# Kernel optimization log

Measured on AMD Instinct MI355X. Metric: run time of the kernel, lower is better.

## Reference

```python
import jax, jax.numpy as jnp
import numpy as np

N_NODES = 10000
N_EDGES = 160000
IN_CH = 1030
HID = 256
HEADS = 4
OUT_CH = 49
NEG_SLOPE = 0.2
EPS = 1e-5


def setup_inputs() -> dict:
    key = jax.random.key(0)
    ks = jax.random.split(key, 20)
    HC = HID * HEADS  # 1024
    inp = {
        "x": jax.random.normal(ks[0], (N_NODES, IN_CH), dtype=jnp.float32),
        "edge_index": jax.random.randint(ks[1], (2, N_EDGES), 0, N_NODES, dtype=jnp.int64),
        # conv1 (GATv2): lin_l (source), lin_r (target), att, out bias
        "c1_wl": jax.random.normal(ks[2], (IN_CH, HC), dtype=jnp.float32) * 0.03,
        "c1_bl": jnp.zeros((HC,), dtype=jnp.float32),
        "c1_wr": jax.random.normal(ks[3], (IN_CH, HC), dtype=jnp.float32) * 0.03,
        "c1_br": jnp.zeros((HC,), dtype=jnp.float32),
        "c1_att": jax.random.normal(ks[4], (HEADS, HID), dtype=jnp.float32) * 0.06,
        "c1_bias": jnp.zeros((HC,), dtype=jnp.float32),
        # norm1 (per-node LayerNorm over channels)
        "ln1_w": jnp.ones((HC,), dtype=jnp.float32),
        "ln1_b": jnp.zeros((HC,), dtype=jnp.float32),
        # conv2
        "c2_wl": jax.random.normal(ks[5], (HC, HC), dtype=jnp.float32) * 0.03,
        "c2_bl": jnp.zeros((HC,), dtype=jnp.float32),
        "c2_wr": jax.random.normal(ks[6], (HC, HC), dtype=jnp.float32) * 0.03,
        "c2_br": jnp.zeros((HC,), dtype=jnp.float32),
        "c2_att": jax.random.normal(ks[7], (HEADS, HID), dtype=jnp.float32) * 0.06,
        "c2_bias": jnp.zeros((HC,), dtype=jnp.float32),
        # norm2
        "ln2_w": jnp.ones((HC,), dtype=jnp.float32),
        "ln2_b": jnp.zeros((HC,), dtype=jnp.float32),
        # classifier: Linear(HC, HID) -> ELU -> Linear(HID, OUT_CH)
        "cls_w1": jax.random.normal(ks[8], (HC, HID), dtype=jnp.float32) * 0.03,
        "cls_b1": jnp.zeros((HID,), dtype=jnp.float32),
        "cls_w2": jax.random.normal(ks[9], (HID, OUT_CH), dtype=jnp.float32) * 0.06,
        "cls_b2": jnp.zeros((OUT_CH,), dtype=jnp.float32),
    }
    return inp


def gatv2_conv(x, src, dst, wl, bl, wr, br, att, bias, n_nodes):
    """PyG GATv2Conv, concat heads. src/dst include self loops."""
    H, C = att.shape
    xl = (x @ wl + bl).reshape(-1, H, C)  # source transform [N,H,C]
    xr = (x @ wr + br).reshape(-1, H, C)  # target transform [N,H,C]
    m = xl[src] + xr[dst]                  # [E,H,C] gather + add
    e = jnp.einsum("ehc,hc->eh", jax.nn.leaky_relu(m, NEG_SLOPE), att)  # [E,H]
    # segment softmax over destination node
    emax = jax.ops.segment_max(e, dst, num_segments=n_nodes)
    p = jnp.exp(e - emax[dst])
    denom = jax.ops.segment_sum(p, dst, num_segments=n_nodes)
    alpha = p / (denom[dst] + 1e-16)       # [E,H]
    out = jax.ops.segment_sum(xl[src] * alpha[:, :, None], dst, num_segments=n_nodes)
    return out.reshape(n_nodes, H * C) + bias


def layer_norm(x, w, b):
    mu = jnp.mean(x, axis=-1, keepdims=True)
    var = jnp.var(x, axis=-1, keepdims=True)
    return (x - mu) / jnp.sqrt(var + EPS) * w + b


def reference(x, edge_index, c1_wl, c1_bl, c1_wr, c1_br, c1_att, c1_bias,
              ln1_w, ln1_b, c2_wl, c2_bl, c2_wr, c2_br, c2_att, c2_bias,
              ln2_w, ln2_b, cls_w1, cls_b1, cls_w2, cls_b2):
    n = x.shape[0]
    loops = jnp.arange(n, dtype=edge_index.dtype)
    src = jnp.concatenate([edge_index[0], loops])  # add_self_loops=True
    dst = jnp.concatenate([edge_index[1], loops])

    h = gatv2_conv(x, src, dst, c1_wl, c1_bl, c1_wr, c1_br, c1_att, c1_bias, n)
    h = jax.nn.elu(layer_norm(h, ln1_w, ln1_b))
    # dropout: identity at inference
    h = gatv2_conv(h, src, dst, c2_wl, c2_bl, c2_wr, c2_br, c2_att, c2_bias, n)
    h = jax.nn.elu(layer_norm(h, ln2_w, ln2_b))
    h = jax.nn.elu(h @ cls_w1 + cls_b1)
    return h @ cls_w2 + cls_b2  # [N, 49]
```

## Files before the change

### kernel.cpp

```cpp
#include <hip/hip_runtime.h>
#include <stdint.h>

#define N_NODES 10000
#define N_EDGES 160000
#define E_TOT   170000
#define IN_CH   1030
#define HC      1024
#define OUT_CH  49
#define NEG_SLOPE 0.2f
#define LN_EPS 1e-5f
#define LOG2E 1.4426950408889634f

#define MPAD  10112
#define K1PAD 1088

typedef __attribute__((ext_vector_type(8))) __bf16 bf16x8;
typedef __attribute__((ext_vector_type(4))) float floatx4;
typedef __attribute__((ext_vector_type(2))) float floatx2;
typedef _Float16 h2 __attribute__((ext_vector_type(2)));

static __device__ __forceinline__ unsigned short f2bf(float f) {
  union { float f; uint32_t u; } v; v.f = f;
  uint32_t u = v.u;
  u += 0x7fffu + ((u >> 16) & 1u);
  return (unsigned short)(u >> 16);
}
static __device__ __forceinline__ unsigned short f2h(float f) {
  _Float16 h = (_Float16)f;
  union { _Float16 h; unsigned short u; } v; v.h = h; return v.u;
}
static __device__ __forceinline__ h2 bits2h2(uint32_t u) {
  union { uint32_t i; h2 h; } v; v.i = u; return v.h;
}
static __device__ __forceinline__ floatx2 h2f2(h2 a) {
  floatx2 r; r.x = (float)a.x; r.y = (float)a.y; return r;
}


__global__ void cast_x_kernel(const float* __restrict__ x, unsigned short* __restrict__ xa,
                              int* __restrict__ counts, int* __restrict__ cursor) {
  int idx = blockIdx.x * 256 + threadIdx.x;
  if (idx < N_NODES) { counts[idx] = 0; cursor[idx] = 0; }
  if (idx >= N_NODES * K1PAD) return;
  int m = idx / K1PAD, k = idx - m * K1PAD;
  float v = (k < IN_CH) ? x[m * IN_CH + k] : 0.f;
  xa[idx] = f2bf(v);
}

__global__ void transpose_cast_kernel(const float* __restrict__ wa, const float* __restrict__ wb,
                                      int split, int lda, int ldb,
                                      int Kvalid, int Kout, unsigned short* __restrict__ out) {
  __shared__ float tile[32][33];
  int n0 = blockIdx.x * 32, k0 = blockIdx.y * 32;
  int tx = threadIdx.x, ty = threadIdx.y;
#pragma unroll
  for (int i = 0; i < 4; i++) {
    int k = k0 + ty + i * 8;
    int n = n0 + tx;
    float v = 0.f;
    if (k < Kvalid) v = (n < split) ? wa[(size_t)k * lda + n] : wb[(size_t)k * ldb + (n - split)];
    tile[ty + i * 8][tx] = v;
  }
  __syncthreads();
#pragma unroll
  for (int i = 0; i < 4; i++) {
    int n = n0 + ty + i * 8;
    int k = k0 + tx;
    out[(size_t)n * Kout + k] = f2bf(tile[tx][ty + i * 8]);
  }
}


__global__ void count_kernel(const int* __restrict__ dstArr, int* __restrict__ counts) {
  int e = blockIdx.x * 256 + threadIdx.x;
  if (e >= E_TOT) return;
  int d = (e < N_EDGES) ? dstArr[e] : (e - N_EDGES);
  atomicAdd(&counts[d], 1);
}

__global__ __launch_bounds__(256) void scan_kernel(const int* __restrict__ counts,
                                                   int* __restrict__ rstart) {
  __shared__ int sm[256];
  int t = threadIdx.x;
  int b0 = t * 40;
  int b1 = b0 + 40; if (b1 > N_NODES) b1 = N_NODES; if (b0 > N_NODES) b0 = N_NODES;
  int s = 0;
  for (int i = b0; i < b1; i++) s += counts[i];
  sm[t] = s; __syncthreads();
  for (int st = 1; st < 256; st <<= 1) {
    int add = (t >= st) ? sm[t - st] : 0;
    __syncthreads();
    sm[t] += add;
    __syncthreads();
  }
  int run = sm[t] - s;
  for (int i = b0; i < b1; i++) { rstart[i] = run; run += counts[i]; }
  if (t == 255) rstart[N_NODES] = run;
}

__global__ void scatter_kernel(const int* __restrict__ srcArr, const int* __restrict__ dstArr,
                               const int* __restrict__ row_start,
                               int* __restrict__ cursor, int* __restrict__ csrsrc) {
  int e = blockIdx.x * 256 + threadIdx.x;
  if (e >= E_TOT) return;
  int d, sv;
  if (e < N_EDGES) { d = dstArr[e]; sv = srcArr[e]; }
  else { d = e - N_EDGES; sv = d; }
  int pos = atomicAdd(&cursor[d], 1);
  csrsrc[row_start[d] + pos] = sv;
}

template <int MODE, int KC>
__global__ __launch_bounds__(256, 4) void gemm_bf16(
    const unsigned short* __restrict__ A, const unsigned short* __restrict__ Bt,
    float* __restrict__ Cf, unsigned short* __restrict__ Cb,
    const float* __restrict__ blo, const float* __restrict__ bhi,
    int M, int ldc, int bsplit)
{
  __shared__ __align__(16) unsigned short As[128 * 64];
  __shared__ __align__(16) unsigned short Bs[128 * 64];
  const int t = threadIdx.x;
  const int w = t >> 6, lane = t & 63;
  const int tile_n = blockIdx.x * 128, tile_m = blockIdx.y * 128;

  floatx4 acc[4][4] = {};

  const int q = w * 64 + lane;
  const int row0 = q >> 3;
  const int gj = (q & 7) ^ (row0 & 7);
  const unsigned short* gA0 = A  + (size_t)(tile_m + row0) * KC + gj * 8;
  const unsigned short* gB0 = Bt + (size_t)(tile_n + row0) * KC + gj * 8;

  const int wm = (w >> 1) * 64, wn = (w & 1) * 64;
  const int lrow = lane & 15, cg0 = (lane >> 4);
  const int sw = lrow & 7;

#pragma unroll 1
  for (int k0 = 0; k0 < KC; k0 += 64) {
#pragma unroll
    for (int p = 0; p < 4; p++) {
      __builtin_amdgcn_global_load_lds(
          (const __attribute__((address_space(1))) void*)(gA0 + p * 32 * KC),
          (__attribute__((address_space(3))) void*)(As + p * 2048 + w * 512), 16, 0, 0);
      __builtin_amdgcn_global_load_lds(
          (const __attribute__((address_space(1))) void*)(gB0 + p * 32 * KC),
          (__attribute__((address_space(3))) void*)(Bs + p * 2048 + w * 512), 16, 0, 0);
    }
    gA0 += 64; gB0 += 64;
    __syncthreads();
#pragma unroll
    for (int h = 0; h < 2; h++) {
      const int sc = (h * 4 + cg0) ^ sw;
      bf16x8 a[4], b[4];
#pragma unroll
      for (int mi = 0; mi < 4; mi++)
        a[mi] = *(const bf16x8*)(As + (wm + mi * 16 + lrow) * 64 + sc * 8);
#pragma unroll
      for (int ni = 0; ni < 4; ni++)
        b[ni] = *(const bf16x8*)(Bs + (wn + ni * 16 + lrow) * 64 + sc * 8);
#pragma unroll
      for (int mi = 0; mi < 4; mi++)
#pragma unroll
        for (int ni = 0; ni < 4; ni++)
          acc[mi][ni] = __builtin_amdgcn_mfma_f32_16x16x32_bf16(a[mi], b[ni], acc[mi][ni], 0, 0, 0);
    }
    __syncthreads();
  }

  const int rbase = (lane >> 4) * 4;
#pragma unroll
  for (int mi = 0; mi < 4; mi++) {
#pragma unroll
    for (int r = 0; r < 4; r++) {
      int m = tile_m + wm + mi * 16 + rbase + r;
      if (m >= M) continue;
#pragma unroll
      for (int ni = 0; ni < 4; ni++) {
        int n = tile_n + wn + ni * 16 + lrow;
        float v = acc[mi][ni][r] + (n < bsplit ? blo[n] : bhi[n - bsplit]);
        if (MODE == 0) {
          Cf[(size_t)m * ldc + n] = v;
        } else if (MODE == 1) {
          Cf[(size_t)m * ldc + n] = v > 0.f ? v : expm1f(v);
        } else {
          Cb[(size_t)m * 2048 + n] = f2h(v);
        }
      }
    }
  }
}


__global__ __launch_bounds__(256) void gat_ln_kernel(
    const unsigned short* __restrict__ xlr,
    const float* __restrict__ att,
    const int* __restrict__ csrsrc, const int* __restrict__ rstart,
    const float* __restrict__ bias,
    const float* __restrict__ lnw, const float* __restrict__ lnb,
    unsigned short* __restrict__ out)
{
  const int d = blockIdx.x;
  const int t = threadIdx.x;
  const int lane = t & 63, wv = t >> 6;
  const int c = wv * 256 + lane * 4;

  uint2 xru = *(const uint2*)(xlr + (size_t)d * 2048 + 1024 + c);
  h2 xr0 = bits2h2(xru.x), xr1 = bits2h2(xru.y);
  float4 aw4 = *(const float4*)(att + c);
  h2 aw0, aw1;
  aw0.x = (_Float16)(aw4.x * LOG2E); aw0.y = (_Float16)(aw4.y * LOG2E);
  aw1.x = (_Float16)(aw4.z * LOG2E); aw1.y = (_Float16)(aw4.w * LOG2E);
  const h2 ns = {(_Float16)NEG_SLOPE, (_Float16)NEG_SLOPE};
  const unsigned short* xbase = xlr + c;

  int start = rstart[d], deg = rstart[d + 1] - start;

  float m = -3.0e38f, l = 0.f;
  floatx2 accA = {0.f, 0.f}, accB = {0.f, 0.f};

  int i = 0;
  for (; i + 4 <= deg; i += 4) {
    int s0 = csrsrc[start + i],     s1 = csrsrc[start + i + 1];
    int s2 = csrsrc[start + i + 2], s3 = csrsrc[start + i + 3];
    uint2 u0 = *(const uint2*)(xbase + (size_t)s0 * 2048);
    uint2 u1 = *(const uint2*)(xbase + (size_t)s1 * 2048);
    uint2 u2 = *(const uint2*)(xbase + (size_t)s2 * 2048);
    uint2 u3 = *(const uint2*)(xbase + (size_t)s3 * 2048);
    h2 xh0a = bits2h2(u0.x), xh0b = bits2h2(u0.y);
    h2 xh1a = bits2h2(u1.x), xh1b = bits2h2(u1.y);
    h2 xh2a = bits2h2(u2.x), xh2b = bits2h2(u2.y);
    h2 xh3a = bits2h2(u3.x), xh3b = bits2h2(u3.y);
    h2 t0a = xh0a + xr0, t0b = xh0b + xr1;
    h2 t1a = xh1a + xr0, t1b = xh1b + xr1;
    h2 t2a = xh2a + xr0, t2b = xh2b + xr1;
    h2 t3a = xh3a + xr0, t3b = xh3b + xr1;
    h2 r0a = __builtin_elementwise_max(t0a, t0a * ns);
    h2 r0b = __builtin_elementwise_max(t0b, t0b * ns);
    h2 r1a = __builtin_elementwise_max(t1a, t1a * ns);
    h2 r1b = __builtin_elementwise_max(t1b, t1b * ns);
    h2 r2a = __builtin_elementwise_max(t2a, t2a * ns);
    h2 r2b = __builtin_elementwise_max(t2b, t2b * ns);
    h2 r3a = __builtin_elementwise_max(t3a, t3a * ns);
    h2 r3b = __builtin_elementwise_max(t3b, t3b * ns);
    float p0 = __builtin_amdgcn_fdot2(r0b, aw1, __builtin_amdgcn_fdot2(r0a, aw0, 0.f, false), false);
    float p1 = __builtin_amdgcn_fdot2(r1b, aw1, __builtin_amdgcn_fdot2(r1a, aw0, 0.f, false), false);
    float p2 = __builtin_amdgcn_fdot2(r2b, aw1, __builtin_amdgcn_fdot2(r2a, aw0, 0.f, false), false);
    float p3 = __builtin_amdgcn_fdot2(r3b, aw1, __builtin_amdgcn_fdot2(r3a, aw0, 0.f, false), false);
#pragma unroll
    for (int mm = 32; mm >= 1; mm >>= 1) {
      p0 += __shfl_xor(p0, mm, 64);
      p1 += __shfl_xor(p1, mm, 64);
      p2 += __shfl_xor(p2, mm, 64);
      p3 += __shfl_xor(p3, mm, 64);
    }
    float mx = fmaxf(fmaxf(p0, p1), fmaxf(p2, p3));
    if (mx > m) {
      float sc = exp2f(m - mx);
      floatx2 scv; scv.x = sc; scv.y = sc;
      accA *= scv; accB *= scv; l *= sc;
      m = mx;
    }
    float pe0 = exp2f(p0 - m), pe1 = exp2f(p1 - m);
    float pe2 = exp2f(p2 - m), pe3 = exp2f(p3 - m);
    floatx2 x0A = h2f2(xh0a), x0B = h2f2(xh0b);
    floatx2 x1A = h2f2(xh1a), x1B = h2f2(xh1b);
    floatx2 x2A = h2f2(xh2a), x2B = h2f2(xh2b);
    floatx2 x3A = h2f2(xh3a), x3B = h2f2(xh3b);
    floatx2 v0; v0.x = pe0; v0.y = pe0;
    floatx2 v1; v1.x = pe1; v1.y = pe1;
    floatx2 v2; v2.x = pe2; v2.y = pe2;
    floatx2 v3; v3.x = pe3; v3.y = pe3;
    accA += x0A * v0; accA += x1A * v1; accA += x2A * v2; accA += x3A * v3;
    accB += x0B * v0; accB += x1B * v1; accB += x2B * v2; accB += x3B * v3;
    l += pe0 + pe1 + pe2 + pe3;
  }
  for (; i < deg; i++) {
    int s0 = csrsrc[start + i];
    uint2 u0 = *(const uint2*)(xbase + (size_t)s0 * 2048);
    h2 xh0a = bits2h2(u0.x), xh0b = bits2h2(u0.y);
    h2 t0a = xh0a + xr0, t0b = xh0b + xr1;
    h2 r0a = __builtin_elementwise_max(t0a, t0a * ns);
    h2 r0b = __builtin_elementwise_max(t0b, t0b * ns);
    float p0 = __builtin_amdgcn_fdot2(r0b, aw1, __builtin_amdgcn_fdot2(r0a, aw0, 0.f, false), false);
#pragma unroll
    for (int mm = 32; mm >= 1; mm >>= 1) p0 += __shfl_xor(p0, mm, 64);
    if (p0 > m) {
      float sc = exp2f(m - p0);
      floatx2 scv; scv.x = sc; scv.y = sc;
      accA *= scv; accB *= scv; l *= sc;
      m = p0;
    }
    float pe0 = exp2f(p0 - m);
    floatx2 x0A = h2f2(xh0a), x0B = h2f2(xh0b);
    floatx2 pe0v; pe0v.x = pe0; pe0v.y = pe0;
    accA += x0A * pe0v;
    accB += x0B * pe0v;
    l += pe0;
  }

  float rd = 1.f / (l + 1e-16f);
  float4 bv = *(const float4*)(bias + c);
  float o0 = accA.x * rd + bv.x, o1 = accA.y * rd + bv.y;
  float o2 = accB.x * rd + bv.z, o3 = accB.y * rd + bv.w;

  __shared__ float ws1[4], ws2[4];
  float s1 = o0 + o1 + o2 + o3;
  float s2 = o0 * o0 + o1 * o1 + o2 * o2 + o3 * o3;
#pragma unroll
  for (int mm = 32; mm >= 1; mm >>= 1) {
    s1 += __shfl_xor(s1, mm, 64);
    s2 += __shfl_xor(s2, mm, 64);
  }
  if (lane == 0) { ws1[wv] = s1; ws2[wv] = s2; }
  __syncthreads();
  float mean = (ws1[0] + ws1[1] + ws1[2] + ws1[3]) * (1.f / 1024.f);
  float var  = (ws2[0] + ws2[1] + ws2[2] + ws2[3]) * (1.f / 1024.f) - mean * mean;
  float rstd = rsqrtf(var + LN_EPS);
  float4 wv4 = *(const float4*)(lnw + c);
  float4 bb  = *(const float4*)(lnb + c);
  float z0 = (o0 - mean) * rstd * wv4.x + bb.x; z0 = z0 > 0.f ? z0 : expm1f(z0);
  float z1 = (o1 - mean) * rstd * wv4.y + bb.y; z1 = z1 > 0.f ? z1 : expm1f(z1);
  float z2 = (o2 - mean) * rstd * wv4.z + bb.z; z2 = z2 > 0.f ? z2 : expm1f(z2);
  float z3 = (o3 - mean) * rstd * wv4.w + bb.w; z3 = z3 > 0.f ? z3 : expm1f(z3);
  ushort4 u;
  u.x = f2bf(z0); u.y = f2bf(z1); u.z = f2bf(z2); u.w = f2bf(z3);
  *(ushort4*)(out + (size_t)d * 1024 + c) = u;
}


__global__ __launch_bounds__(64) void cls2_kernel(
    const float* __restrict__ h3, const float* __restrict__ w2,
    const float* __restrict__ b2, float* __restrict__ out)
{
  __shared__ float row[256];
  int node = blockIdx.x, t = threadIdx.x;
  *(float4*)(row + t * 4) = *(const float4*)(h3 + (size_t)node * 256 + t * 4);
  __syncthreads();
  if (t < OUT_CH) {
    float a0 = 0.f, a1 = 0.f, a2 = 0.f, a3 = 0.f;
#pragma unroll 4
    for (int k = 0; k < 256; k += 4) {
      float4 r = *(const float4*)(row + k);
      a0 += r.x * w2[(k + 0) * OUT_CH + t];
      a1 += r.y * w2[(k + 1) * OUT_CH + t];
      a2 += r.z * w2[(k + 2) * OUT_CH + t];
      a3 += r.w * w2[(k + 3) * OUT_CH + t];
    }
    out[node * OUT_CH + t] = (a0 + a1) + (a2 + a3) + b2[t];
  }
}


extern "C" void kernel_launch(void* const* d_in, const int* in_sizes, int n_in,
                              void* d_out, int out_size, void* d_ws, size_t ws_size,
                              hipStream_t stream)
{
  const float* x       = (const float*)d_in[0];
  const int*   ei      = (const int*)d_in[1];
  const float* c1_wl   = (const float*)d_in[2];
  const float* c1_bl   = (const float*)d_in[3];
  const float* c1_wr   = (const float*)d_in[4];
  const float* c1_br   = (const float*)d_in[5];
  const float* c1_att  = (const float*)d_in[6];
  const float* c1_bias = (const float*)d_in[7];
  const float* ln1_w   = (const float*)d_in[8];
  const float* ln1_b   = (const float*)d_in[9];
  const float* c2_wl   = (const float*)d_in[10];
  const float* c2_bl   = (const float*)d_in[11];
  const float* c2_wr   = (const float*)d_in[12];
  const float* c2_br   = (const float*)d_in[13];
  const float* c2_att  = (const float*)d_in[14];
  const float* c2_bias = (const float*)d_in[15];
  const float* ln2_w   = (const float*)d_in[16];
  const float* ln2_b   = (const float*)d_in[17];
  const float* cls_w1  = (const float*)d_in[18];
  const float* cls_b1  = (const float*)d_in[19];
  const float* cls_w2  = (const float*)d_in[20];
  const float* cls_b2  = (const float*)d_in[21];

  const int* srcArr = ei;
  const int* dstArr = ei + N_EDGES;

  char* ws = (char*)d_ws;
  size_t off = 0;
  auto alloc = [&](size_t bytes) { void* p = ws + off; off += (bytes + 255) & ~(size_t)255; return p; };
  unsigned short* xa      = (unsigned short*)alloc((size_t)MPAD * K1PAD * 2);
  unsigned short* wt1     = (unsigned short*)alloc((size_t)2048 * K1PAD * 2);
  unsigned short* wt2     = (unsigned short*)alloc((size_t)2048 * 1024 * 2);
  unsigned short* wtc1    = (unsigned short*)alloc((size_t)256 * 1024 * 2);
  unsigned short* xlr     = (unsigned short*)alloc((size_t)N_NODES * 2048 * 2);
  float*          h3      = (float*)alloc((size_t)N_NODES * 256 * 4);
  unsigned short* hb      = (unsigned short*)alloc((size_t)MPAD * 1024 * 2);
  int*            counts  = (int*)alloc(N_NODES * 4);
  int*            cursor  = (int*)alloc(N_NODES * 4);
  int*            rstart  = (int*)alloc((N_NODES + 1) * 4);
  int*            csrsrc  = (int*)alloc(E_TOT * 4);
  (void)in_sizes; (void)n_in; (void)out_size; (void)ws_size;

  cast_x_kernel<<<(N_NODES * K1PAD + 255) / 256, 256, 0, stream>>>(x, xa, counts, cursor);
  transpose_cast_kernel<<<dim3(64, 34), dim3(32, 8), 0, stream>>>(c1_wl, c1_wr, 1024, 1024, 1024, IN_CH, K1PAD, wt1);
  transpose_cast_kernel<<<dim3(64, 32), dim3(32, 8), 0, stream>>>(c2_wl, c2_wr, 1024, 1024, 1024, 1024, 1024, wt2);
  transpose_cast_kernel<<<dim3(8, 32), dim3(32, 8), 0, stream>>>(cls_w1, cls_w1, 256, 256, 256, 1024, 1024, wtc1);

  count_kernel<<<(E_TOT + 255) / 256, 256, 0, stream>>>(dstArr, counts);
  scan_kernel<<<1, 256, 0, stream>>>(counts, rstart);
  scatter_kernel<<<(E_TOT + 255) / 256, 256, 0, stream>>>(srcArr, dstArr, rstart, cursor, csrsrc);

  gemm_bf16<2, K1PAD><<<dim3(16, 79), 256, 0, stream>>>(xa, wt1, nullptr, xlr, c1_bl, c1_br, N_NODES, 0, 1024);
  gat_ln_kernel<<<N_NODES, 256, 0, stream>>>(xlr, c1_att, csrsrc, rstart, c1_bias, ln1_w, ln1_b, hb);

  gemm_bf16<2, 1024><<<dim3(16, 79), 256, 0, stream>>>(hb, wt2, nullptr, xlr, c2_bl, c2_br, N_NODES, 0, 1024);
  gat_ln_kernel<<<N_NODES, 256, 0, stream>>>(xlr, c2_att, csrsrc, rstart, c2_bias, ln2_w, ln2_b, hb);

  gemm_bf16<1, 1024><<<dim3(2, 79), 256, 0, stream>>>(hb, wtc1, h3, nullptr, cls_b1, cls_b1, N_NODES, 256, 1024);
  cls2_kernel<<<N_NODES, 64, 0, stream>>>(h3, cls_w2, cls_b2, (float*)d_out);
}
```

Baseline: 500.3 us.

## Process four edges in parallel per wavefront with 16-lane groups in GAT aggregation

Restructures the GATv2 aggregation+LayerNorm kernel so that each wavefront splits into four 16-lane groups. Each group handles a different edge, and each lane covers 16 channels with 128-bit loads instead of 4 channels with 64-bit loads. This shortens the per-edge cross-lane reduction from 6 to 4 shuffle steps and prefetches the next source index. Groups run independent online softmaxes that are merged with shuffles at the end, and only group 0 writes the output. The cost is higher register use (16 accumulators per lane), a final merge step, and divergence on the rescale branch.

```diff
diff --git a/kernel.cpp b/kernel.cpp
--- a/kernel.cpp
+++ b/kernel.cpp
@@ -202,129 +202,166 @@
   const int d = blockIdx.x;
   const int t = threadIdx.x;
   const int lane = t & 63, wv = t >> 6;
-  const int c = wv * 256 + lane * 4;
-
-  uint2 xru = *(const uint2*)(xlr + (size_t)d * 2048 + 1024 + c);
-  h2 xr0 = bits2h2(xru.x), xr1 = bits2h2(xru.y);
-  float4 aw4 = *(const float4*)(att + c);
-  h2 aw0, aw1;
-  aw0.x = (_Float16)(aw4.x * LOG2E); aw0.y = (_Float16)(aw4.y * LOG2E);
-  aw1.x = (_Float16)(aw4.z * LOG2E); aw1.y = (_Float16)(aw4.w * LOG2E);
+  const int g  = lane >> 4;
+  const int li = lane & 15;
+  const int c = wv * 256 + li * 16;
+
+  const unsigned short* xrp = xlr + (size_t)d * 2048 + 1024 + c;
+  uint4 xru0 = *(const uint4*)(xrp);
+  uint4 xru1 = *(const uint4*)(xrp + 8);
+  h2 xr[8];
+  xr[0] = bits2h2(xru0.x); xr[1] = bits2h2(xru0.y);
+  xr[2] = bits2h2(xru0.z); xr[3] = bits2h2(xru0.w);
+  xr[4] = bits2h2(xru1.x); xr[5] = bits2h2(xru1.y);
+  xr[6] = bits2h2(xru1.z); xr[7] = bits2h2(xru1.w);
+
+  float4 a0 = *(const float4*)(att + c);
+  float4 a1 = *(const float4*)(att + c + 4);
+  float4 a2 = *(const float4*)(att + c + 8);
+  float4 a3 = *(const float4*)(att + c + 12);
+  h2 aw[8];
+  aw[0].x = (_Float16)(a0.x * LOG2E); aw[0].y = (_Float16)(a0.y * LOG2E);
+  aw[1].x = (_Float16)(a0.z * LOG2E); aw[1].y = (_Float16)(a0.w * LOG2E);
+  aw[2].x = (_Float16)(a1.x * LOG2E); aw[2].y = (_Float16)(a1.y * LOG2E);
+  aw[3].x = (_Float16)(a1.z * LOG2E); aw[3].y = (_Float16)(a1.w * LOG2E);
+  aw[4].x = (_Float16)(a2.x * LOG2E); aw[4].y = (_Float16)(a2.y * LOG2E);
+  aw[5].x = (_Float16)(a2.z * LOG2E); aw[5].y = (_Float16)(a2.w * LOG2E);
+  aw[6].x = (_Float16)(a3.x * LOG2E); aw[6].y = (_Float16)(a3.y * LOG2E);
+  aw[7].x = (_Float16)(a3.z * LOG2E); aw[7].y = (_Float16)(a3.w * LOG2E);
   const h2 ns = {(_Float16)NEG_SLOPE, (_Float16)NEG_SLOPE};
+
   const unsigned short* xbase = xlr + c;
-
-  int start = rstart[d], deg = rstart[d + 1] - start;
+  const int start = rstart[d], end = rstart[d + 1];
 
   float m = -3.0e38f, l = 0.f;
-  floatx2 accA = {0.f, 0.f}, accB = {0.f, 0.f};
-
-  int i = 0;
-  for (; i + 4 <= deg; i += 4) {
-    int s0 = csrsrc[start + i],     s1 = csrsrc[start + i + 1];
-    int s2 = csrsrc[start + i + 2], s3 = csrsrc[start + i + 3];
-    uint2 u0 = *(const uint2*)(xbase + (size_t)s0 * 2048);
-    uint2 u1 = *(const uint2*)(xbase + (size_t)s1 * 2048);
-    uint2 u2 = *(const uint2*)(xbase + (size_t)s2 * 2048);
-    uint2 u3 = *(const uint2*)(xbase + (size_t)s3 * 2048);
-    h2 xh0a = bits2h2(u0.x), xh0b = bits2h2(u0.y);
-    h2 xh1a = bits2h2(u1.x), xh1b = bits2h2(u1.y);
-    h2 xh2a = bits2h2(u2.x), xh2b = bits2h2(u2.y);
-    h2 xh3a = bits2h2(u3.x), xh3b = bits2h2(u3.y);
-    h2 t0a = xh0a + xr0, t0b = xh0b + xr1;
-    h2 t1a = xh1a + xr0, t1b = xh1b + xr1;
-    h2 t2a = xh2a + xr0, t2b = xh2b + xr1;
-    h2 t3a = xh3a + xr0, t3b = xh3b + xr1;
-    h2 r0a = __builtin_elementwise_max(t0a, t0a * ns);
-    h2 r0b = __builtin_elementwise_max(t0b, t0b * ns);
-    h2 r1a = __builtin_elementwise_max(t1a, t1a * ns);
-    h2 r1b = __builtin_elementwise_max(t1b, t1b * ns);
-    h2 r2a = __builtin_elementwise_max(t2a, t2a * ns);
-    h2 r2b = __builtin_elementwise_max(t2b, t2b * ns);
-    h2 r3a = __builtin_elementwise_max(t3a, t3a * ns);
-    h2 r3b = __builtin_elementwise_max(t3b, t3b * ns);
-    float p0 = __builtin_amdgcn_fdot2(r0b, aw1, __builtin_amdgcn_fdot2(r0a, aw0, 0.f, false), false);
-    float p1 = __builtin_amdgcn_fdot2(r1b, aw1, __builtin_amdgcn_fdot2(r1a, aw0, 0.f, false), false);
-    float p2 = __builtin_amdgcn_fdot2(r2b, aw1, __builtin_amdgcn_fdot2(r2a, aw0, 0.f, false), false);
-    float p3 = __builtin_amdgcn_fdot2(r3b, aw1, __builtin_amdgcn_fdot2(r3a, aw0, 0.f, false), false);
-#pragma unroll
-    for (int mm = 32; mm >= 1; mm >>= 1) {
-      p0 += __shfl_xor(p0, mm, 64);
-      p1 += __shfl_xor(p1, mm, 64);
-      p2 += __shfl_xor(p2, mm, 64);
-      p3 += __shfl_xor(p3, mm, 64);
-    }
-    float mx = fmaxf(fmaxf(p0, p1), fmaxf(p2, p3));
-    if (mx > m) {
-      float sc = exp2f(m - mx);
+  floatx2 acc[8] = {};
+
+  int eq0 = start + g;
+  int s_next = csrsrc[(eq0 < end) ? eq0 : start];
+
+  for (int i = start; i < end; i += 4) {
+    const int scur = s_next;
+    const bool valid = (i + g) < end;
+    const int eqn = i + 4 + g;
+    s_next = csrsrc[(eqn < end) ? eqn : start];
+
+    const unsigned short* xp = xbase + (size_t)scur * 2048;
+    uint4 u0 = *(const uint4*)(xp);
+    uint4 u1 = *(const uint4*)(xp + 8);
+    h2 xh[8];
+    xh[0] = bits2h2(u0.x); xh[1] = bits2h2(u0.y);
+    xh[2] = bits2h2(u0.z); xh[3] = bits2h2(u0.w);
+    xh[4] = bits2h2(u1.x); xh[5] = bits2h2(u1.y);
+    xh[6] = bits2h2(u1.z); xh[7] = bits2h2(u1.w);
+
+    float pa = 0.f, pb = 0.f;
+#pragma unroll
+    for (int j = 0; j < 4; j++) {
+      h2 tj = xh[j] + xr[j];
+      h2 rj = __builtin_elementwise_max(tj, tj * ns);
+      pa = __builtin_amdgcn_fdot2(rj, aw[j], pa, false);
+      h2 tk = xh[j + 4] + xr[j + 4];
+      h2 rk = __builtin_elementwise_max(tk, tk * ns);
+      pb = __builtin_amdgcn_fdot2(rk, aw[j + 4], pb, false);
+    }
+    float p = pa + pb;
+    p += __shfl_xor(p, 1, 64);
+    p += __shfl_xor(p, 2, 64);
+    p += __shfl_xor(p, 4, 64);
+    p += __shfl_xor(p, 8, 64);
+
+    const float mnew = fmaxf(m, p);
+    const float pe = valid ? exp2f(p - mnew) : 0.f;
+    if (__any(valid && (p > m))) {
+      const float sc = exp2f(m - mnew);
       floatx2 scv; scv.x = sc; scv.y = sc;
-      accA *= scv; accB *= scv; l *= sc;
-      m = mx;
-    }
-    float pe0 = exp2f(p0 - m), pe1 = exp2f(p1 - m);
-    float pe2 = exp2f(p2 - m), pe3 = exp2f(p3 - m);
-    floatx2 x0A = h2f2(xh0a), x0B = h2f2(xh0b);
-    floatx2 x1A = h2f2(xh1a), x1B = h2f2(xh1b);
-    floatx2 x2A = h2f2(xh2a), x2B = h2f2(xh2b);
-    floatx2 x3A = h2f2(xh3a), x3B = h2f2(xh3b);
-    floatx2 v0; v0.x = pe0; v0.y = pe0;
-    floatx2 v1; v1.x = pe1; v1.y = pe1;
-    floatx2 v2; v2.x = pe2; v2.y = pe2;
-    floatx2 v3; v3.x = pe3; v3.y = pe3;
-    accA += x0A * v0; accA += x1A * v1; accA += x2A * v2; accA += x3A * v3;
-    accB += x0B * v0; accB += x1B * v1; accB += x2B * v2; accB += x3B * v3;
-    l += pe0 + pe1 + pe2 + pe3;
-  }
-  for (; i < deg; i++) {
-    int s0 = csrsrc[start + i];
-    uint2 u0 = *(const uint2*)(xbase + (size_t)s0 * 2048);
-    h2 xh0a = bits2h2(u0.x), xh0b = bits2h2(u0.y);
-    h2 t0a = xh0a + xr0, t0b = xh0b + xr1;
-    h2 r0a = __builtin_elementwise_max(t0a, t0a * ns);
-    h2 r0b = __builtin_elementwise_max(t0b, t0b * ns);
-    float p0 = __builtin_amdgcn_fdot2(r0b, aw1, __builtin_amdgcn_fdot2(r0a, aw0, 0.f, false), false);
-#pragma unroll
-    for (int mm = 32; mm >= 1; mm >>= 1) p0 += __shfl_xor(p0, mm, 64);
-    if (p0 > m) {
-      float sc = exp2f(m - p0);
-      floatx2 scv; scv.x = sc; scv.y = sc;
-      accA *= scv; accB *= scv; l *= sc;
-      m = p0;
-    }
-    float pe0 = exp2f(p0 - m);
-    floatx2 x0A = h2f2(xh0a), x0B = h2f2(xh0b);
-    floatx2 pe0v; pe0v.x = pe0; pe0v.y = pe0;
-    accA += x0A * pe0v;
-    accB += x0B * pe0v;
-    l += pe0;
-  }
-
-  float rd = 1.f / (l + 1e-16f);
-  float4 bv = *(const float4*)(bias + c);
-  float o0 = accA.x * rd + bv.x, o1 = accA.y * rd + bv.y;
-  float o2 = accB.x * rd + bv.z, o3 = accB.y * rd + bv.w;
+#pragma unroll
+      for (int j = 0; j < 8; j++) acc[j] *= scv;
+      l *= sc;
+      m = mnew;
+    }
+#pragma unroll
+    for (int j = 0; j < 8; j++) {
+      acc[j].x += (float)xh[j].x * pe;
+      acc[j].y += (float)xh[j].y * pe;
+    }
+    l += pe;
+  }
+
+  float M = m;
+  M = fmaxf(M, __shfl_xor(M, 16, 64));
+  M = fmaxf(M, __shfl_xor(M, 32, 64));
+  const float sc = exp2f(m - M);
+  l *= sc;
+  l += __shfl_xor(l, 16, 64);
+  l += __shfl_xor(l, 32, 64);
+  floatx2 scv; scv.x = sc; scv.y = sc;
+#pragma unroll
+  for (int j = 0; j < 8; j++) {
+    acc[j] *= scv;
+    acc[j].x += __shfl_xor(acc[j].x, 16, 64);
+    acc[j].y += __shfl_xor(acc[j].y, 16, 64);
+    acc[j].x += __shfl_xor(acc[j].x, 32, 64);
+    acc[j].y += __shfl_xor(acc[j].y, 32, 64);
+  }
+
+  const float rd = 1.f / (l + 1e-16f);
+  float4 b0 = *(const float4*)(bias + c);
+  float4 b1 = *(const float4*)(bias + c + 4);
+  float4 b2 = *(const float4*)(bias + c + 8);
+  float4 b3 = *(const float4*)(bias + c + 12);
+  float o[16];
+  o[0]  = acc[0].x * rd + b0.x; o[1]  = acc[0].y * rd + b0.y;
+  o[2]  = acc[1].x * rd + b0.z; o[3]  = acc[1].y * rd + b0.w;
+  o[4]  = acc[2].x * rd + b1.x; o[5]  = acc[2].y * rd + b1.y;
+  o[6]  = acc[3].x * rd + b1.z; o[7]  = acc[3].y * rd + b1.w;
+  o[8]  = acc[4].x * rd + b2.x; o[9]  = acc[4].y * rd + b2.y;
+  o[10] = acc[5].x * rd + b2.z; o[11] = acc[5].y * rd + b2.w;
+  o[12] = acc[6].x * rd + b3.x; o[13] = acc[6].y * rd + b3.y;
+  o[14] = acc[7].x * rd + b3.z; o[15] = acc[7].y * rd + b3.w;
 
   __shared__ float ws1[4], ws2[4];
-  float s1 = o0 + o1 + o2 + o3;
-  float s2 = o0 * o0 + o1 * o1 + o2 * o2 + o3 * o3;
-#pragma unroll
-  for (int mm = 32; mm >= 1; mm >>= 1) {
-    s1 += __shfl_xor(s1, mm, 64);
-    s2 += __shfl_xor(s2, mm, 64);
-  }
+  float s1 = 0.f, s2 = 0.f;
+#pragma unroll
+  for (int j = 0; j < 16; j++) { s1 += o[j]; s2 += o[j] * o[j]; }
+  s1 += __shfl_xor(s1, 1, 64); s2 += __shfl_xor(s2, 1, 64);
+  s1 += __shfl_xor(s1, 2, 64); s2 += __shfl_xor(s2, 2, 64);
+  s1 += __shfl_xor(s1, 4, 64); s2 += __shfl_xor(s2, 4, 64);
+  s1 += __shfl_xor(s1, 8, 64); s2 += __shfl_xor(s2, 8, 64);
   if (lane == 0) { ws1[wv] = s1; ws2[wv] = s2; }
   __syncthreads();
-  float mean = (ws1[0] + ws1[1] + ws1[2] + ws1[3]) * (1.f / 1024.f);
-  float var  = (ws2[0] + ws2[1] + ws2[2] + ws2[3]) * (1.f / 1024.f) - mean * mean;
-  float rstd = rsqrtf(var + LN_EPS);
-  float4 wv4 = *(const float4*)(lnw + c);
-  float4 bb  = *(const float4*)(lnb + c);
-  float z0 = (o0 - mean) * rstd * wv4.x + bb.x; z0 = z0 > 0.f ? z0 : expm1f(z0);
-  float z1 = (o1 - mean) * rstd * wv4.y + bb.y; z1 = z1 > 0.f ? z1 : expm1f(z1);
-  float z2 = (o2 - mean) * rstd * wv4.z + bb.z; z2 = z2 > 0.f ? z2 : expm1f(z2);
-  float z3 = (o3 - mean) * rstd * wv4.w + bb.w; z3 = z3 > 0.f ? z3 : expm1f(z3);
-  ushort4 u;
-  u.x = f2bf(z0); u.y = f2bf(z1); u.z = f2bf(z2); u.w = f2bf(z3);
-  *(ushort4*)(out + (size_t)d * 1024 + c) = u;
+  const float mean = (ws1[0] + ws1[1] + ws1[2] + ws1[3]) * (1.f / 1024.f);
+  const float var  = (ws2[0] + ws2[1] + ws2[2] + ws2[3]) * (1.f / 1024.f) - mean * mean;
+  const float rstd = rsqrtf(var + LN_EPS);
+
+  if (g == 0) {
+    float4 w0 = *(const float4*)(lnw + c);
+    float4 w1 = *(const float4*)(lnw + c + 4);
+    float4 w2 = *(const float4*)(lnw + c + 8);
+    float4 w3 = *(const float4*)(lnw + c + 12);
+    float4 q0 = *(const float4*)(lnb + c);
+    float4 q1 = *(const float4*)(lnb + c + 4);
+    float4 q2 = *(const float4*)(lnb + c + 8);
+    float4 q3 = *(const float4*)(lnb + c + 12);
+    float lw[16] = {w0.x,w0.y,w0.z,w0.w, w1.x,w1.y,w1.z,w1.w,
+                    w2.x,w2.y,w2.z,w2.w, w3.x,w3.y,w3.z,w3.w};
+    float lb[16] = {q0.x,q0.y,q0.z,q0.w, q1.x,q1.y,q1.z,q1.w,
+                    q2.x,q2.y,q2.z,q2.w, q3.x,q3.y,q3.z,q3.w};
+    uint32_t zz[16];
+#pragma unroll
+    for (int j = 0; j < 16; j++) {
+      float z = (o[j] - mean) * rstd * lw[j] + lb[j];
+      z = z > 0.f ? z : expm1f(z);
+      zz[j] = (uint32_t)f2bf(z);
+    }
+    uint4 v0, v1;
+    v0.x = zz[0]  | (zz[1]  << 16); v0.y = zz[2]  | (zz[3]  << 16);
+    v0.z = zz[4]  | (zz[5]  << 16); v0.w = zz[6]  | (zz[7]  << 16);
+    v1.x = zz[8]  | (zz[9]  << 16); v1.y = zz[10] | (zz[11] << 16);
+    v1.z = zz[12] | (zz[13] << 16); v1.w = zz[14] | (zz[15] << 16);
+    *(uint4*)(out + (size_t)d * 1024 + c) = v0;
+    *(uint4*)(out + (size_t)d * 1024 + c + 8) = v1;
+  }
 }
 
 
```

Result: slower. 550.2 us (+10.0%).

## Software-pipeline GAT neighbor gathers and remap GEMM workgroups per XCD

Applied to the files above, without the earlier changes.

The GAT aggregation loop now prefetches the next group of neighbor feature rows and the index group after that, overlapping gather latency with the softmax and accumulate math. The CSR index array is padded with 16 zeroed entries so the look-ahead reads stay in bounds. The GEMM workgroup-to-tile mapping is remapped so that blocks sharing an XCD get contiguous tiles, to improve L2 locality. This adds register pressure and some redundant prefetch loads at the tail.

```diff
diff --git a/kernel.cpp b/kernel.cpp
--- a/kernel.cpp
+++ b/kernel.cpp
@@ -102,7 +102,10 @@
                                const int* __restrict__ row_start,
                                int* __restrict__ cursor, int* __restrict__ csrsrc) {
   int e = blockIdx.x * 256 + threadIdx.x;
-  if (e >= E_TOT) return;
+  if (e >= E_TOT) {
+    return;
+  }
+  if (e < 16) csrsrc[E_TOT + e] = 0;
   int d, sv;
   if (e < N_EDGES) { d = dstArr[e]; sv = srcArr[e]; }
   else { d = e - N_EDGES; sv = d; }
@@ -121,13 +124,19 @@
   __shared__ __align__(16) unsigned short Bs[128 * 64];
   const int t = threadIdx.x;
   const int w = t >> 6, lane = t & 63;
-  const int tile_n = blockIdx.x * 128, tile_m = blockIdx.y * 128;
+
+  const unsigned int nwg = gridDim.x * gridDim.y;
+  const unsigned int bid = blockIdx.y * gridDim.x + blockIdx.x;
+  const unsigned int q8 = nwg >> 3, r8 = nwg & 7;
+  const unsigned int xcd = bid & 7, sub = bid >> 3;
+  const unsigned int wg = (xcd < r8 ? xcd * (q8 + 1) : r8 * (q8 + 1) + (xcd - r8) * q8) + sub;
+  const int tile_n = (wg % gridDim.x) * 128, tile_m = (wg / gridDim.x) * 128;
 
   floatx4 acc[4][4] = {};
 
-  const int q = w * 64 + lane;
-  const int row0 = q >> 3;
-  const int gj = (q & 7) ^ (row0 & 7);
+  const int qq = w * 64 + lane;
+  const int row0 = qq >> 3;
+  const int gj = (qq & 7) ^ (row0 & 7);
   const unsigned short* gA0 = A  + (size_t)(tile_m + row0) * KC + gj * 8;
   const unsigned short* gB0 = Bt + (size_t)(tile_n + row0) * KC + gj * 8;
 
@@ -219,60 +228,74 @@
   floatx2 accA = {0.f, 0.f}, accB = {0.f, 0.f};
 
   int i = 0;
-  for (; i + 4 <= deg; i += 4) {
-    int s0 = csrsrc[start + i],     s1 = csrsrc[start + i + 1];
-    int s2 = csrsrc[start + i + 2], s3 = csrsrc[start + i + 3];
-    uint2 u0 = *(const uint2*)(xbase + (size_t)s0 * 2048);
-    uint2 u1 = *(const uint2*)(xbase + (size_t)s1 * 2048);
-    uint2 u2 = *(const uint2*)(xbase + (size_t)s2 * 2048);
-    uint2 u3 = *(const uint2*)(xbase + (size_t)s3 * 2048);
-    h2 xh0a = bits2h2(u0.x), xh0b = bits2h2(u0.y);
-    h2 xh1a = bits2h2(u1.x), xh1b = bits2h2(u1.y);
-    h2 xh2a = bits2h2(u2.x), xh2b = bits2h2(u2.y);
-    h2 xh3a = bits2h2(u3.x), xh3b = bits2h2(u3.y);
-    h2 t0a = xh0a + xr0, t0b = xh0b + xr1;
-    h2 t1a = xh1a + xr0, t1b = xh1b + xr1;
-    h2 t2a = xh2a + xr0, t2b = xh2b + xr1;
-    h2 t3a = xh3a + xr0, t3b = xh3b + xr1;
-    h2 r0a = __builtin_elementwise_max(t0a, t0a * ns);
-    h2 r0b = __builtin_elementwise_max(t0b, t0b * ns);
-    h2 r1a = __builtin_elementwise_max(t1a, t1a * ns);
-    h2 r1b = __builtin_elementwise_max(t1b, t1b * ns);
-    h2 r2a = __builtin_elementwise_max(t2a, t2a * ns);
-    h2 r2b = __builtin_elementwise_max(t2b, t2b * ns);
-    h2 r3a = __builtin_elementwise_max(t3a, t3a * ns);
-    h2 r3b = __builtin_elementwise_max(t3b, t3b * ns);
-    float p0 = __builtin_amdgcn_fdot2(r0b, aw1, __builtin_amdgcn_fdot2(r0a, aw0, 0.f, false), false);
-    float p1 = __builtin_amdgcn_fdot2(r1b, aw1, __builtin_amdgcn_fdot2(r1a, aw0, 0.f, false), false);
-    float p2 = __builtin_amdgcn_fdot2(r2b, aw1, __builtin_amdgcn_fdot2(r2a, aw0, 0.f, false), false);
-    float p3 = __builtin_amdgcn_fdot2(r3b, aw1, __builtin_amdgcn_fdot2(r3a, aw0, 0.f, false), false);
-#pragma unroll
-    for (int mm = 32; mm >= 1; mm >>= 1) {
-      p0 += __shfl_xor(p0, mm, 64);
-      p1 += __shfl_xor(p1, mm, 64);
-      p2 += __shfl_xor(p2, mm, 64);
-      p3 += __shfl_xor(p3, mm, 64);
-    }
-    float mx = fmaxf(fmaxf(p0, p1), fmaxf(p2, p3));
-    if (mx > m) {
-      float sc = exp2f(m - mx);
-      floatx2 scv; scv.x = sc; scv.y = sc;
-      accA *= scv; accB *= scv; l *= sc;
-      m = mx;
-    }
-    float pe0 = exp2f(p0 - m), pe1 = exp2f(p1 - m);
-    float pe2 = exp2f(p2 - m), pe3 = exp2f(p3 - m);
-    floatx2 x0A = h2f2(xh0a), x0B = h2f2(xh0b);
-    floatx2 x1A = h2f2(xh1a), x1B = h2f2(xh1b);
-    floatx2 x2A = h2f2(xh2a), x2B = h2f2(xh2b);
-    floatx2 x3A = h2f2(xh3a), x3B = h2f2(xh3b);
-    floatx2 v0; v0.x = pe0; v0.y = pe0;
-    floatx2 v1; v1.x = pe1; v1.y = pe1;
-    floatx2 v2; v2.x = pe2; v2.y = pe2;
-    floatx2 v3; v3.x = pe3; v3.y = pe3;
-    accA += x0A * v0; accA += x1A * v1; accA += x2A * v2; accA += x3A * v3;
-    accB += x0B * v0; accB += x1B * v1; accB += x2B * v2; accB += x3B * v3;
-    l += pe0 + pe1 + pe2 + pe3;
+  if (deg >= 4) {
+    int sA0 = csrsrc[start],     sA1 = csrsrc[start + 1];
+    int sA2 = csrsrc[start + 2], sA3 = csrsrc[start + 3];
+    uint2 uA0 = *(const uint2*)(xbase + (size_t)sA0 * 2048);
+    uint2 uA1 = *(const uint2*)(xbase + (size_t)sA1 * 2048);
+    uint2 uA2 = *(const uint2*)(xbase + (size_t)sA2 * 2048);
+    uint2 uA3 = *(const uint2*)(xbase + (size_t)sA3 * 2048);
+    int sB0 = csrsrc[start + 4], sB1 = csrsrc[start + 5];
+    int sB2 = csrsrc[start + 6], sB3 = csrsrc[start + 7];
+    for (; i + 4 <= deg; i += 4) {
+      int sC0 = csrsrc[start + i + 8],  sC1 = csrsrc[start + i + 9];
+      int sC2 = csrsrc[start + i + 10], sC3 = csrsrc[start + i + 11];
+      uint2 uB0 = *(const uint2*)(xbase + (size_t)sB0 * 2048);
+      uint2 uB1 = *(const uint2*)(xbase + (size_t)sB1 * 2048);
+      uint2 uB2 = *(const uint2*)(xbase + (size_t)sB2 * 2048);
+      uint2 uB3 = *(const uint2*)(xbase + (size_t)sB3 * 2048);
+
+      h2 xh0a = bits2h2(uA0.x), xh0b = bits2h2(uA0.y);
+      h2 xh1a = bits2h2(uA1.x), xh1b = bits2h2(uA1.y);
+      h2 xh2a = bits2h2(uA2.x), xh2b = bits2h2(uA2.y);
+      h2 xh3a = bits2h2(uA3.x), xh3b = bits2h2(uA3.y);
+      h2 t0a = xh0a + xr0, t0b = xh0b + xr1;
+      h2 t1a = xh1a + xr0, t1b = xh1b + xr1;
+      h2 t2a = xh2a + xr0, t2b = xh2b + xr1;
+      h2 t3a = xh3a + xr0, t3b = xh3b + xr1;
+      h2 r0a = __builtin_elementwise_max(t0a, t0a * ns);
+      h2 r0b = __builtin_elementwise_max(t0b, t0b * ns);
+      h2 r1a = __builtin_elementwise_max(t1a, t1a * ns);
+      h2 r1b = __builtin_elementwise_max(t1b, t1b * ns);
+      h2 r2a = __builtin_elementwise_max(t2a, t2a * ns);
+      h2 r2b = __builtin_elementwise_max(t2b, t2b * ns);
+      h2 r3a = __builtin_elementwise_max(t3a, t3a * ns);
+      h2 r3b = __builtin_elementwise_max(t3b, t3b * ns);
+      float p0 = __builtin_amdgcn_fdot2(r0b, aw1, __builtin_amdgcn_fdot2(r0a, aw0, 0.f, false), false);
+      float p1 = __builtin_amdgcn_fdot2(r1b, aw1, __builtin_amdgcn_fdot2(r1a, aw0, 0.f, false), false);
+      float p2 = __builtin_amdgcn_fdot2(r2b, aw1, __builtin_amdgcn_fdot2(r2a, aw0, 0.f, false), false);
+      float p3 = __builtin_amdgcn_fdot2(r3b, aw1, __builtin_amdgcn_fdot2(r3a, aw0, 0.f, false), false);
+#pragma unroll
+      for (int mm = 32; mm >= 1; mm >>= 1) {
+        p0 += __shfl_xor(p0, mm, 64);
+        p1 += __shfl_xor(p1, mm, 64);
+        p2 += __shfl_xor(p2, mm, 64);
+        p3 += __shfl_xor(p3, mm, 64);
+      }
+      float mx = fmaxf(fmaxf(p0, p1), fmaxf(p2, p3));
+      if (mx > m) {
+        float sc = exp2f(m - mx);
+        floatx2 scv; scv.x = sc; scv.y = sc;
+        accA *= scv; accB *= scv; l *= sc;
+        m = mx;
+      }
+      float pe0 = exp2f(p0 - m), pe1 = exp2f(p1 - m);
+      float pe2 = exp2f(p2 - m), pe3 = exp2f(p3 - m);
+      floatx2 x0A = h2f2(xh0a), x0B = h2f2(xh0b);
+      floatx2 x1A = h2f2(xh1a), x1B = h2f2(xh1b);
+      floatx2 x2A = h2f2(xh2a), x2B = h2f2(xh2b);
+      floatx2 x3A = h2f2(xh3a), x3B = h2f2(xh3b);
+      floatx2 v0; v0.x = pe0; v0.y = pe0;
+      floatx2 v1; v1.x = pe1; v1.y = pe1;
+      floatx2 v2; v2.x = pe2; v2.y = pe2;
+      floatx2 v3; v3.x = pe3; v3.y = pe3;
+      accA += x0A * v0; accA += x1A * v1; accA += x2A * v2; accA += x3A * v3;
+      accB += x0B * v0; accB += x1B * v1; accB += x2B * v2; accB += x3B * v3;
+      l += pe0 + pe1 + pe2 + pe3;
+
+      uA0 = uB0; uA1 = uB1; uA2 = uB2; uA3 = uB3;
+      sB0 = sC0; sB1 = sC1; sB2 = sC2; sB3 = sC3;
+    }
   }
   for (; i < deg; i++) {
     int s0 = csrsrc[start + i];
@@ -394,7 +417,7 @@
   int*            counts  = (int*)alloc(N_NODES * 4);
   int*            cursor  = (int*)alloc(N_NODES * 4);
   int*            rstart  = (int*)alloc((N_NODES + 1) * 4);
-  int*            csrsrc  = (int*)alloc(E_TOT * 4);
+  int*            csrsrc  = (int*)alloc((E_TOT + 16) * 4);
   (void)in_sizes; (void)n_in; (void)out_size; (void)ws_size;
 
   cast_x_kernel<<<(N_NODES * K1PAD + 255) / 256, 256, 0, stream>>>(x, xa, counts, cursor);
```

Result: no change. 496.5 us (-0.8%).
